# Performance work log

Hardware: AMD Instinct MI355X
Metric: run time of the kernel (lower is better)

The kernel has to match this reference:

```python
import jax, jax.numpy as jnp
import numpy as np
import math

LN_EPS = 1e-5

def layer_norm(x, g, b):
    m = jnp.mean(x, axis=-1, keepdims=True)
    v = jnp.mean((x - m) ** 2, axis=-1, keepdims=True)
    return (x - m) / jnp.sqrt(v + LN_EPS) * g + b

def setup_inputs() -> dict:
    key = jax.random.key(0)
    ks = jax.random.split(key, 8)
    B, H, W, C = 64, 24, 24, 768   # ViT-B/16 @ 384 -> 576 tokens
    SD, N = 512, 8192              # sd_dim, FDT codebook size
    ft = jax.random.normal(ks[0], (B, H, W, C), jnp.float32)
    sd = jax.random.normal(ks[1], (N, SD), jnp.float32)
    mask = jax.random.randint(ks[2], (B, H * W), 0, 2, jnp.int32)
    inp = {
        "ft": ft,
        "sd": sd,
        "mask": mask,
        "ln1_g": jnp.ones((C,), jnp.float32),
        "ln1_b": jnp.zeros((C,), jnp.float32),
        "w1": jax.random.normal(ks[3], (C, SD), jnp.float32) * 0.02,
        "b1": jnp.zeros((SD,), jnp.float32),
        "ln2_g": jnp.ones((SD,), jnp.float32),
        "ln2_b": jnp.zeros((SD,), jnp.float32),
        "w2": jax.random.normal(ks[4], (SD, SD), jnp.float32) * 0.02,
        "b2": jnp.zeros((SD,), jnp.float32),
    }
    return inp

def reference(ft, sd, mask, ln1_g, ln1_b, w1, b1, ln2_g, ln2_b, w2, b2):
    B, H, W, C = ft.shape
    temperature = 1.0
    x = ft.reshape(B, H * W, C)                     # [B, T, C]
    # q_map: LN -> Linear -> GELU (exact, torch default) -> LN -> Linear
    q = layer_norm(x, ln1_g, ln1_b)
    q = q @ w1 + b1
    q = jax.nn.gelu(q, approximate=False)
    q = layer_norm(q, ln2_g, ln2_b)
    q = q @ w2 + b2                                  # [B, T, SD]
    att_dim = sd.shape[1]
    inner = jnp.einsum('btd,nd->btn', q, sd)         # [B, T, N]
    inner = inner / math.sqrt(att_dim)
    m = (mask == 0).astype(inner.dtype)              # [B, T]
    inner = inner * m[:, :, None]
    inner = inner / temperature
    pooled = inner.sum(axis=1)                       # sum pool over tokens -> [B, N]
    att_weight = jax.nn.softmax(pooled, axis=-1)     # [B, N]
    att_ft = att_weight @ sd                         # [B, SD]
    return (att_weight, att_ft, sd)
```

## Files before the change

kernel.cpp:

```cpp
#include <hip/hip_runtime.h>
#include <math.h>

typedef unsigned short u16;
typedef _Float16 half4 __attribute__((ext_vector_type(4)));
typedef _Float16 half8 __attribute__((ext_vector_type(8)));
typedef float f32x4 __attribute__((ext_vector_type(4)));
typedef u16 u16x8 __attribute__((ext_vector_type(8)));

#define B_ 64
#define T_ 576
#define C_ 768
#define SD_ 512
#define N_ 8192
#define TOK_ (B_*T_)
#define MT_ 5
#define HROWS_ 640

__device__ __forceinline__ u16 f2h(float x) {
    _Float16 v = (_Float16)x;
    return __builtin_bit_cast(u16, v);
}

__global__ void zero_kernel(unsigned int* attwh_u, unsigned int* qpad_u, int* count) {
    int i = blockIdx.x * 256 + threadIdx.x;
    if (i < 524288) attwh_u[i] = 0u;
    if (i < 16384)  qpad_u[i]  = 0u;
    if (i < 64)     count[i]   = 0;
}

__global__ __launch_bounds__(256) void transpose_cvt_kernel(
    const float* __restrict__ src, const float* __restrict__ g,
    u16* __restrict__ dst, int K, int N)
{
    __shared__ float tile[64][65];
    int k0 = blockIdx.x * 64, n0 = blockIdx.y * 64;
    int tid = threadIdx.x;
#pragma unroll
    for (int p = 0; p < 16; p++) {
        int idx = p * 256 + tid;
        int r = idx >> 6, c = idx & 63;
        float gv = g ? g[k0 + r] : 1.0f;
        tile[r][c] = src[(size_t)(k0 + r) * N + n0 + c] * gv;
    }
    __syncthreads();
#pragma unroll
    for (int p = 0; p < 16; p++) {
        int idx = p * 256 + tid;
        int r = idx >> 6, c = idx & 63;
        dst[(size_t)(n0 + r) * K + k0 + c] = f2h(tile[c][r]);
    }
}

__global__ void cvt_plain_kernel(const float* __restrict__ src, u16* __restrict__ dst) {
    int i = blockIdx.x * 256 + threadIdx.x;
    const f32x4* s = (const f32x4*)(src + (size_t)i * 8);
    f32x4 a = s[0], b = s[1];
    u16x8 o;
    o[0]=f2h(a[0]); o[1]=f2h(a[1]); o[2]=f2h(a[2]); o[3]=f2h(a[3]);
    o[4]=f2h(b[0]); o[5]=f2h(b[1]); o[6]=f2h(b[2]); o[7]=f2h(b[3]);
    *(u16x8*)(dst + (size_t)i * 8) = o;
}

__global__ void fold_bias_kernel(const float* __restrict__ w, const float* __restrict__ bvec,
                                 const float* __restrict__ beta, float* __restrict__ outp,
                                 int K, int N)
{
    int n = blockIdx.x, l = threadIdx.x;
    float s = 0.f;
    for (int k = l; k < K; k += 64) s += beta[k] * w[(size_t)k * N + n];
#pragma unroll
    for (int o = 32; o > 0; o >>= 1) s += __shfl_xor(s, o);
    if (l == 0) outp[n] = bvec[n] + s;
}

__global__ void compact_kernel(const int* __restrict__ mask, int* __restrict__ list,
                               int* __restrict__ count) {
    int g = blockIdx.x * 256 + threadIdx.x;
    if (g >= TOK_) return;
    int b = g / T_, t = g % T_;
    if (mask[g] == 0) {
        int slot = atomicAdd(&count[b], 1);
        list[b * T_ + slot] = t;
    }
}

__global__ void ln1_stats_kernel(const float* __restrict__ ft, const int* __restrict__ list,
                                 const int* __restrict__ count, float2* __restrict__ stats1) {
    int wv = threadIdx.x >> 6, lane = threadIdx.x & 63;
    int s = blockIdx.x * 4 + wv;
    int b = s / T_, slot = s % T_;
    if (slot >= count[b]) return;
    int t = list[b * T_ + slot];
    const float4* row = (const float4*)(ft + (size_t)(b * T_ + t) * C_);
    float sum = 0.f, sq = 0.f;
#pragma unroll
    for (int p = 0; p < 3; p++) {
        float4 v = row[lane + 64 * p];
        sum += (v.x + v.y) + (v.z + v.w);
        sq  += v.x * v.x + v.y * v.y + v.z * v.z + v.w * v.w;
    }
#pragma unroll
    for (int o = 32; o > 0; o >>= 1) { sum += __shfl_xor(sum, o); sq += __shfl_xor(sq, o); }
    if (lane == 0) {
        float mu  = sum * (1.0f / C_);
        float var = fmaxf(sq * (1.0f / C_) - mu * mu, 0.0f);
        stats1[b * T_ + slot] = make_float2(mu, 1.0f / sqrtf(var + 1e-5f));
    }
}

__global__ __launch_bounds__(256) void gemm1_kernel(
    const float* __restrict__ ft, const u16* __restrict__ w1T,
    const float* __restrict__ b1p, const int* __restrict__ list,
    const int* __restrict__ count, const float2* __restrict__ stats1,
    u16* __restrict__ h)
{
    const int b = blockIdx.x / MT_, mt = blockIdx.x % MT_;
    const int cnt = count[b];
    const int row0 = mt * 128;
    if (row0 >= cnt) return;
    const int n0 = blockIdx.y * 128;

    __shared__ __align__(16) u16 As[128 * 64];
    __shared__ __align__(16) u16 Bs[128 * 64];
    __shared__ float rmu[128], rrs[128];
    __shared__ int rtok[128];

    const int tid = threadIdx.x;
    if (tid < 128) {
        int slot = row0 + tid;
        bool v = slot < cnt;
        rtok[tid] = v ? list[b * T_ + slot] : 0;
        float2 st = v ? stats1[b * T_ + slot] : make_float2(0.f, 0.f);
        rmu[tid] = v ? st.x : 0.f;
        rrs[tid] = v ? st.y : 0.f;
    }
    __syncthreads();

    const float* aptr[4]; float amu[4], ars[4]; int adst[4];
    const u16* bptr[4];
#pragma unroll
    for (int it = 0; it < 4; it++) {
        int c = it * 256 + tid, r = c >> 3, q = c & 7;
        aptr[it] = ft + (size_t)(b * T_ + rtok[r]) * C_ + q * 8;
        amu[it] = rmu[r]; ars[it] = rrs[r];
        adst[it] = r * 64 + ((q ^ (r & 7)) << 3);
        bptr[it] = w1T + (size_t)(n0 + r) * C_ + q * 8;
    }

    const int lane = tid & 63, w = tid >> 6;
    const int wm = w >> 1, wn = w & 1;
    const int lr = lane & 15, lg = lane >> 4;
    int arow[4], brow[4];
#pragma unroll
    for (int i = 0; i < 4; i++) { arow[i] = wm * 64 + i * 16 + lr; brow[i] = wn * 64 + i * 16 + lr; }

    f32x4 pa0[4], pa1[4]; u16x8 pb[4];
#pragma unroll
    for (int it = 0; it < 4; it++) {
        pa0[it] = *(const f32x4*)(aptr[it]);
        pa1[it] = *(const f32x4*)(aptr[it] + 4);
        pb[it]  = *(const u16x8*)(bptr[it]);
    }

    f32x4 acc[4][4] = {};
    const int NKT = C_ / 64;
    for (int kt = 0; kt < NKT; kt++) {
        __syncthreads();
#pragma unroll
        for (int it = 0; it < 4; it++) {
            float mu = amu[it], rs = ars[it];
            u16x8 o;
            o[0] = f2h((pa0[it][0] - mu) * rs);
            o[1] = f2h((pa0[it][1] - mu) * rs);
            o[2] = f2h((pa0[it][2] - mu) * rs);
            o[3] = f2h((pa0[it][3] - mu) * rs);
            o[4] = f2h((pa1[it][0] - mu) * rs);
            o[5] = f2h((pa1[it][1] - mu) * rs);
            o[6] = f2h((pa1[it][2] - mu) * rs);
            o[7] = f2h((pa1[it][3] - mu) * rs);
            *(u16x8*)&As[adst[it]] = o;
            *(u16x8*)&Bs[adst[it]] = pb[it];
        }
        __syncthreads();
        if (kt + 1 < NKT) {
            int k = (kt + 1) * 64;
#pragma unroll
            for (int it = 0; it < 4; it++) {
                pa0[it] = *(const f32x4*)(aptr[it] + k);
                pa1[it] = *(const f32x4*)(aptr[it] + k + 4);
                pb[it]  = *(const u16x8*)(bptr[it] + k);
            }
        }
#pragma unroll
        for (int ks = 0; ks < 4; ks++) {
            int kq = ks * 4 + lg;
            int qo = kq >> 1, ho = (kq & 1) << 2;
            half4 aF[4], bF[4];
#pragma unroll
            for (int i = 0; i < 4; i++)
                aF[i] = *(const half4*)&As[arow[i] * 64 + ((qo ^ (arow[i] & 7)) << 3) + ho];
#pragma unroll
            for (int i = 0; i < 4; i++)
                bF[i] = *(const half4*)&Bs[brow[i] * 64 + ((qo ^ (brow[i] & 7)) << 3) + ho];
#pragma unroll
            for (int mi = 0; mi < 4; mi++)
#pragma unroll
                for (int ni = 0; ni < 4; ni++)
                    acc[mi][ni] = __builtin_amdgcn_mfma_f32_16x16x16f16(aF[mi], bF[ni], acc[mi][ni], 0, 0, 0);
        }
    }

    float bb[4];
#pragma unroll
    for (int ni = 0; ni < 4; ni++) bb[ni] = b1p[n0 + wn * 64 + ni * 16 + lr];
#pragma unroll
    for (int mi = 0; mi < 4; mi++) {
#pragma unroll
        for (int r = 0; r < 4; r++) {
            int grow = row0 + wm * 64 + mi * 16 + 4 * lg + r;
            u16* hp = h + (size_t)(b * HROWS_ + grow) * SD_ + n0 + wn * 64 + lr;
#pragma unroll
            for (int ni = 0; ni < 4; ni++) {
                float x = acc[mi][ni][r] + bb[ni];
                float gel = 0.5f * x * (1.0f + erff(x * 0.70710678118654752f));
                hp[ni * 16] = f2h(gel);
            }
        }
    }
}

__global__ void ln2_stats_kernel(const u16* __restrict__ h, const int* __restrict__ count,
                                 float2* __restrict__ stats2) {
    int wv = threadIdx.x >> 6, lane = threadIdx.x & 63;
    int s = blockIdx.x * 4 + wv;
    int b = s / T_, slot = s % T_;
    if (slot >= count[b]) return;
    const half8* row = (const half8*)(h + (size_t)(b * HROWS_ + slot) * SD_);
    half8 v = row[lane];
    float sum = 0.f, sq = 0.f;
#pragma unroll
    for (int j = 0; j < 8; j++) { float f = (float)v[j]; sum += f; sq += f * f; }
#pragma unroll
    for (int o = 32; o > 0; o >>= 1) { sum += __shfl_xor(sum, o); sq += __shfl_xor(sq, o); }
    if (lane == 0) {
        float mu  = sum * (1.0f / SD_);
        float var = fmaxf(sq * (1.0f / SD_) - mu * mu, 0.0f);
        stats2[b * T_ + slot] = make_float2(mu, 1.0f / sqrtf(var + 1e-5f));
    }
}

__global__ __launch_bounds__(256) void gemm2_kernel(
    const u16* __restrict__ h, const u16* __restrict__ w2T,
    const int* __restrict__ count, const float2* __restrict__ stats2,
    float* __restrict__ partial)
{
    const int b = blockIdx.x / MT_, mt = blockIdx.x % MT_;
    const int cnt = count[b];
    const int row0 = mt * 128;
    if (row0 >= cnt) return;
    const int n0 = blockIdx.y * 128;

    __shared__ __align__(16) u16 As[128 * 64];
    __shared__ __align__(16) u16 Bs[128 * 64];
    __shared__ float rmu[128], rrs[128];
    __shared__ float redbuf[4][64];

    const int tid = threadIdx.x;
    if (tid < 128) {
        int slot = row0 + tid;
        bool v = slot < cnt;
        float2 st = v ? stats2[b * T_ + slot] : make_float2(0.f, 0.f);
        rmu[tid] = v ? st.x : 0.f;
        rrs[tid] = v ? st.y : 0.f;
    }
    __syncthreads();

    const u16* aptr[4]; float amu[4], ars[4]; int adst[4];
    const u16* bptr[4];
#pragma unroll
    for (int it = 0; it < 4; it++) {
        int c = it * 256 + tid, r = c >> 3, q = c & 7;
        aptr[it] = h + (size_t)(b * HROWS_ + row0 + r) * SD_ + q * 8;
        amu[it] = rmu[r]; ars[it] = rrs[r];
        adst[it] = r * 64 + ((q ^ (r & 7)) << 3);
        bptr[it] = w2T + (size_t)(n0 + r) * SD_ + q * 8;
    }

    const int lane = tid & 63, w = tid >> 6;
    const int wm = w >> 1, wn = w & 1;
    const int lr = lane & 15, lg = lane >> 4;
    int arow[4], brow[4];
#pragma unroll
    for (int i = 0; i < 4; i++) { arow[i] = wm * 64 + i * 16 + lr; brow[i] = wn * 64 + i * 16 + lr; }

    u16x8 pa[4], pb[4];
#pragma unroll
    for (int it = 0; it < 4; it++) {
        pa[it] = *(const u16x8*)(aptr[it]);
        pb[it] = *(const u16x8*)(bptr[it]);
    }

    f32x4 acc[4][4] = {};
    const int NKT = SD_ / 64;
    for (int kt = 0; kt < NKT; kt++) {
        __syncthreads();
#pragma unroll
        for (int it = 0; it < 4; it++) {
            float mu = amu[it], rs = ars[it];
            half8 hv = __builtin_bit_cast(half8, pa[it]);
            u16x8 o;
#pragma unroll
            for (int j = 0; j < 8; j++) o[j] = f2h(((float)hv[j] - mu) * rs);
            *(u16x8*)&As[adst[it]] = o;
            *(u16x8*)&Bs[adst[it]] = pb[it];
        }
        __syncthreads();
        if (kt + 1 < NKT) {
            int k = (kt + 1) * 64;
#pragma unroll
            for (int it = 0; it < 4; it++) {
                pa[it] = *(const u16x8*)(aptr[it] + k);
                pb[it] = *(const u16x8*)(bptr[it] + k);
            }
        }
#pragma unroll
        for (int ks = 0; ks < 4; ks++) {
            int kq = ks * 4 + lg;
            int qo = kq >> 1, ho = (kq & 1) << 2;
            half4 aF[4], bF[4];
#pragma unroll
            for (int i = 0; i < 4; i++)
                aF[i] = *(const half4*)&As[arow[i] * 64 + ((qo ^ (arow[i] & 7)) << 3) + ho];
#pragma unroll
            for (int i = 0; i < 4; i++)
                bF[i] = *(const half4*)&Bs[brow[i] * 64 + ((qo ^ (brow[i] & 7)) << 3) + ho];
#pragma unroll
            for (int mi = 0; mi < 4; mi++)
#pragma unroll
                for (int ni = 0; ni < 4; ni++)
                    acc[mi][ni] = __builtin_amdgcn_mfma_f32_16x16x16f16(aF[mi], bF[ni], acc[mi][ni], 0, 0, 0);
        }
    }

    float s[4];
#pragma unroll
    for (int ni = 0; ni < 4; ni++) {
        float t = 0.f;
#pragma unroll
        for (int mi = 0; mi < 4; mi++)
#pragma unroll
            for (int r = 0; r < 4; r++) t += acc[mi][ni][r];
        t += __shfl_xor(t, 16);
        t += __shfl_xor(t, 32);
        s[ni] = t;
    }
    if (lane < 16) {
#pragma unroll
        for (int ni = 0; ni < 4; ni++) redbuf[w][ni * 16 + lr] = s[ni];
    }
    __syncthreads();
    if (tid < 128) {
        int wn2 = tid >> 6, idx = tid & 63;
        float v = redbuf[wn2][idx] + redbuf[wn2 + 2][idx];
        partial[(size_t)(b * MT_ + mt) * SD_ + n0 + tid] = v;
    }
}

__global__ void qsum_reduce_kernel(const float* __restrict__ partial, const int* __restrict__ count,
                                   const float* __restrict__ b2p, u16* __restrict__ qsumh) {
    int i = blockIdx.x * 256 + threadIdx.x;
    int b = i >> 9, d = i & 511;
    int cnt = count[b];
    int mts = (cnt + 127) >> 7;
    float s = 0.f;
    for (int mt = 0; mt < mts; mt++) s += partial[(size_t)(b * MT_ + mt) * SD_ + d];
    s = (s + (float)cnt * b2p[d]) * 0.04419417382415922f;
    qsumh[i] = f2h(s);
}

__global__ __launch_bounds__(256) void gemm_plain_kernel(
    const u16* __restrict__ A, int ldA,
    const u16* __restrict__ BT, int ldBT,
    float* __restrict__ C, int ldC, int nkt)
{
    const int kz = blockIdx.x, nt = blockIdx.y;
    const int n0 = nt * 128;
    const int kbase = kz * nkt * 64;

    __shared__ __align__(16) u16 As[128 * 64];
    __shared__ __align__(16) u16 Bs[128 * 64];

    const int tid = threadIdx.x;
    const u16* aptr[4]; const u16* bptr[4]; int adst[4];
#pragma unroll
    for (int it = 0; it < 4; it++) {
        int c = it * 256 + tid, r = c >> 3, q = c & 7;
        aptr[it] = A  + (size_t)r * ldA + kbase + q * 8;
        bptr[it] = BT + (size_t)(n0 + r) * ldBT + kbase + q * 8;
        adst[it] = r * 64 + ((q ^ (r & 7)) << 3);
    }

    const int lane = tid & 63, w = tid >> 6;
    const int wm = w >> 1, wn = w & 1;
    const int lr = lane & 15, lg = lane >> 4;
    int arow[4], brow[4];
#pragma unroll
    for (int i = 0; i < 4; i++) { arow[i] = wm * 64 + i * 16 + lr; brow[i] = wn * 64 + i * 16 + lr; }

    u16x8 pa[4], pb[4];
#pragma unroll
    for (int it = 0; it < 4; it++) {
        pa[it] = *(const u16x8*)(aptr[it]);
        pb[it] = *(const u16x8*)(bptr[it]);
    }

    f32x4 acc[4][4] = {};
    for (int kt = 0; kt < nkt; kt++) {
        __syncthreads();
#pragma unroll
        for (int it = 0; it < 4; it++) {
            *(u16x8*)&As[adst[it]] = pa[it];
            *(u16x8*)&Bs[adst[it]] = pb[it];
        }
        __syncthreads();
        if (kt + 1 < nkt) {
            int k = (kt + 1) * 64;
#pragma unroll
            for (int it = 0; it < 4; it++) {
                pa[it] = *(const u16x8*)(aptr[it] + k);
                pb[it] = *(const u16x8*)(bptr[it] + k);
            }
        }
#pragma unroll
        for (int ks = 0; ks < 4; ks++) {
            int kq = ks * 4 + lg;
            int qo = kq >> 1, ho = (kq & 1) << 2;
            half4 aF[4], bF[4];
#pragma unroll
            for (int i = 0; i < 4; i++)
                aF[i] = *(const half4*)&As[arow[i] * 64 + ((qo ^ (arow[i] & 7)) << 3) + ho];
#pragma unroll
            for (int i = 0; i < 4; i++)
                bF[i] = *(const half4*)&Bs[brow[i] * 64 + ((qo ^ (brow[i] & 7)) << 3) + ho];
#pragma unroll
            for (int mi = 0; mi < 4; mi++)
#pragma unroll
                for (int ni = 0; ni < 4; ni++)
                    acc[mi][ni] = __builtin_amdgcn_mfma_f32_16x16x16f16(aF[mi], bF[ni], acc[mi][ni], 0, 0, 0);
        }
    }

    float* Cb = C + (size_t)kz * 128 * ldC + n0;
#pragma unroll
    for (int mi = 0; mi < 4; mi++)
#pragma unroll
        for (int r = 0; r < 4; r++) {
            int grow = wm * 64 + mi * 16 + 4 * lg + r;
#pragma unroll
            for (int ni = 0; ni < 4; ni++)
                Cb[(size_t)grow * ldC + wn * 64 + ni * 16 + lr] = acc[mi][ni][r];
        }
}

__global__ __launch_bounds__(256) void softmax_kernel(const float* __restrict__ pooled,
                                                      float* __restrict__ attw,
                                                      u16* __restrict__ attwh) {
    __shared__ float rowm[N_];
    __shared__ float red[4];
    int b = blockIdx.x, tid = threadIdx.x;
    const float4* src = (const float4*)(pooled + (size_t)b * N_);
    float mx = -3.4e38f;
#pragma unroll
    for (int p = 0; p < 8; p++) {
        float4 v = src[tid + 256 * p];
        *((float4*)&rowm[(tid + 256 * p) * 4]) = v;
        mx = fmaxf(fmaxf(fmaxf(v.x, v.y), fmaxf(v.z, v.w)), mx);
    }
#pragma unroll
    for (int o = 32; o > 0; o >>= 1) mx = fmaxf(mx, __shfl_xor(mx, o));
    if ((tid & 63) == 0) red[tid >> 6] = mx;
    __syncthreads();
    mx = fmaxf(fmaxf(red[0], red[1]), fmaxf(red[2], red[3]));
    __syncthreads();
    float s = 0.f;
    for (int p = 0; p < 8; p++) {
        int i4 = tid + 256 * p;
        float4 v = *((float4*)&rowm[i4 * 4]);
        v.x = expf(v.x - mx); v.y = expf(v.y - mx);
        v.z = expf(v.z - mx); v.w = expf(v.w - mx);
        *((float4*)&rowm[i4 * 4]) = v;
        s += (v.x + v.y) + (v.z + v.w);
    }
#pragma unroll
    for (int o = 32; o > 0; o >>= 1) s += __shfl_xor(s, o);
    if ((tid & 63) == 0) red[tid >> 6] = s;
    __syncthreads();
    s = ((red[0] + red[1]) + (red[2] + red[3]));
    float inv = 1.0f / s;
    float4* dst = (float4*)(attw + (size_t)b * N_);
    u16* dh = attwh + (size_t)b * N_;
    for (int p = 0; p < 8; p++) {
        int i4 = tid + 256 * p;
        float4 v = *((float4*)&rowm[i4 * 4]);
        v.x *= inv; v.y *= inv; v.z *= inv; v.w *= inv;
        dst[i4] = v;
        ushort4 pk;
        pk.x = f2h(v.x); pk.y = f2h(v.y); pk.z = f2h(v.z); pk.w = f2h(v.w);
        *(ushort4*)(dh + (size_t)i4 * 4) = pk;
    }
}

__global__ void attft_reduce_kernel(const float* __restrict__ p2, float* __restrict__ att_ft) {
    int i = blockIdx.x * 256 + threadIdx.x;
    int b = i >> 9, d = i & 511;
    float s = 0.f;
#pragma unroll
    for (int kz = 0; kz < 8; kz++) s += p2[(size_t)kz * 128 * SD_ + (size_t)b * SD_ + d];
    att_ft[i] = s;
}

extern "C" void kernel_launch(void* const* d_in, const int* in_sizes, int n_in,
                              void* d_out, int out_size, void* d_ws, size_t ws_size,
                              hipStream_t stream) {
    (void)in_sizes; (void)n_in; (void)out_size; (void)ws_size;
    const float* ft  = (const float*)d_in[0];
    const float* sd  = (const float*)d_in[1];
    const int*   mask= (const int*)d_in[2];
    const float* g1  = (const float*)d_in[3];
    const float* bl1 = (const float*)d_in[4];
    const float* w1  = (const float*)d_in[5];
    const float* b1  = (const float*)d_in[6];
    const float* g2  = (const float*)d_in[7];
    const float* bl2 = (const float*)d_in[8];
    const float* w2  = (const float*)d_in[9];
    const float* b2  = (const float*)d_in[10];
    float* out = (float*)d_out;
    char* W = (char*)d_ws;

    u16*    w1T    = (u16*)(W + 0);
    u16*    w2T    = (u16*)(W + 786432);
    u16*    sdh    = (u16*)(W + 1310720);
    u16*    sdT    = (u16*)(W + 9699328);
    float*  b1p    = (float*)(W + 18087936);
    float*  b2p    = (float*)(W + 18089984);
    int*    list   = (int*)(W + 18092032);
    int*    count  = (int*)(W + 18239488);
    float2* st1    = (float2*)(W + 18239744);
    float2* st2    = (float2*)(W + 18534656);
    u16*    h      = (u16*)(W + 18829568);
    float*  partial= (float*)(W + 60772608);
    u16*    qsumh  = (u16*)(W + 61427968);
    float*  pooled = (float*)(W + 61559040);
    u16*    attwh  = (u16*)(W + 65753344);
    float*  p2     = (float*)(W + 67850496);

    float* att_w  = out;
    float* att_ft = out + (size_t)B_ * N_;
    float* sd_out = out + (size_t)B_ * N_ + (size_t)B_ * SD_;

    zero_kernel<<<2048, 256, 0, stream>>>((unsigned int*)attwh, (unsigned int*)(qsumh + 64 * SD_), count);
    transpose_cvt_kernel<<<dim3(C_ / 64, SD_ / 64), 256, 0, stream>>>(w1, g1, w1T, C_, SD_);
    transpose_cvt_kernel<<<dim3(SD_ / 64, SD_ / 64), 256, 0, stream>>>(w2, g2, w2T, SD_, SD_);
    transpose_cvt_kernel<<<dim3(N_ / 64, SD_ / 64), 256, 0, stream>>>(sd, nullptr, sdT, N_, SD_);
    cvt_plain_kernel<<<2048, 256, 0, stream>>>(sd, sdh);
    fold_bias_kernel<<<SD_, 64, 0, stream>>>(w1, b1, bl1, b1p, C_, SD_);
    fold_bias_kernel<<<SD_, 64, 0, stream>>>(w2, b2, bl2, b2p, SD_, SD_);
    compact_kernel<<<144, 256, 0, stream>>>(mask, list, count);
    ln1_stats_kernel<<<TOK_ / 4, 256, 0, stream>>>(ft, list, count, st1);
    gemm1_kernel<<<dim3(B_ * MT_, 4), 256, 0, stream>>>(ft, w1T, b1p, list, count, st1, h);
    ln2_stats_kernel<<<TOK_ / 4, 256, 0, stream>>>(h, count, st2);
    gemm2_kernel<<<dim3(B_ * MT_, 4), 256, 0, stream>>>(h, w2T, count, st2, partial);
    qsum_reduce_kernel<<<128, 256, 0, stream>>>(partial, count, b2p, qsumh);
    gemm_plain_kernel<<<dim3(1, 64), 256, 0, stream>>>(qsumh, SD_, sdh, SD_, pooled, N_, 8);
    softmax_kernel<<<B_, 256, 0, stream>>>(pooled, att_w, attwh);
    gemm_plain_kernel<<<dim3(8, 4), 256, 0, stream>>>(attwh, N_, sdT, N_, p2, SD_, 16);
    attft_reduce_kernel<<<128, 256, 0, stream>>>(p2, att_ft);
    hipMemcpyAsync(sd_out, sd, (size_t)N_ * SD_ * sizeof(float), hipMemcpyDeviceToDevice, stream);
}
```

Measured before the change: 474.6 us.

## Fuse LN2 stats into GEMM1 epilogue, use 16x16x32 MFMA, merge sd prep

GEMM1's epilogue now computes per-row partial sums and sums of squares of the GELU output and writes them to a partials buffer. GEMM2 reduces these 8 partials to get the LayerNorm-2 mean and inverse std, so the separate ln2_stats pass that re-read h is gone. All three GEMM kernels switch from the 16x16x16 f16 MFMA with half4 fragments to the 16x16x32 variant with half8 LDS reads, halving the MFMA issue count and LDS load instructions per k-tile. The sd half conversion and transpose are merged into one kernel that reads sd once. In exchange there are extra shuffles in the GEMM1 epilogue, a larger workspace, and stats computed from fp32 GELU values rather than the fp16-rounded h.

```diff
diff --git a/kernel.cpp b/kernel.cpp
--- a/kernel.cpp
+++ b/kernel.cpp
@@ -2,7 +2,6 @@
 #include <math.h>
 
 typedef unsigned short u16;
-typedef _Float16 half4 __attribute__((ext_vector_type(4)));
 typedef _Float16 half8 __attribute__((ext_vector_type(8)));
 typedef float f32x4 __attribute__((ext_vector_type(4)));
 typedef u16 u16x8 __attribute__((ext_vector_type(8)));
@@ -51,14 +50,27 @@
     }
 }
 
-__global__ void cvt_plain_kernel(const float* __restrict__ src, u16* __restrict__ dst) {
-    int i = blockIdx.x * 256 + threadIdx.x;
-    const f32x4* s = (const f32x4*)(src + (size_t)i * 8);
-    f32x4 a = s[0], b = s[1];
-    u16x8 o;
-    o[0]=f2h(a[0]); o[1]=f2h(a[1]); o[2]=f2h(a[2]); o[3]=f2h(a[3]);
-    o[4]=f2h(b[0]); o[5]=f2h(b[1]); o[6]=f2h(b[2]); o[7]=f2h(b[3]);
-    *(u16x8*)(dst + (size_t)i * 8) = o;
+__global__ __launch_bounds__(256) void sd_prep_kernel(
+    const float* __restrict__ sd, u16* __restrict__ sdh, u16* __restrict__ sdT)
+{
+    __shared__ float tile[64][65];
+    int k0 = blockIdx.x * 64, n0 = blockIdx.y * 64;
+    int tid = threadIdx.x;
+#pragma unroll
+    for (int p = 0; p < 16; p++) {
+        int idx = p * 256 + tid;
+        int r = idx >> 6, c = idx & 63;
+        float v = sd[(size_t)(k0 + r) * SD_ + n0 + c];
+        tile[r][c] = v;
+        sdh[(size_t)(k0 + r) * SD_ + n0 + c] = f2h(v);
+    }
+    __syncthreads();
+#pragma unroll
+    for (int p = 0; p < 16; p++) {
+        int idx = p * 256 + tid;
+        int r = idx >> 6, c = idx & 63;
+        sdT[(size_t)(n0 + r) * N_ + k0 + c] = f2h(tile[c][r]);
+    }
 }
 
 __global__ void fold_bias_kernel(const float* __restrict__ w, const float* __restrict__ bvec,
@@ -112,7 +124,7 @@
     const float* __restrict__ ft, const u16* __restrict__ w1T,
     const float* __restrict__ b1p, const int* __restrict__ list,
     const int* __restrict__ count, const float2* __restrict__ stats1,
-    u16* __restrict__ h)
+    u16* __restrict__ h, float* __restrict__ rstat)
 {
     const int b = blockIdx.x / MT_, mt = blockIdx.x % MT_;
     const int cnt = count[b];
@@ -192,21 +204,23 @@
             }
         }
 #pragma unroll
-        for (int ks = 0; ks < 4; ks++) {
-            int kq = ks * 4 + lg;
-            int qo = kq >> 1, ho = (kq & 1) << 2;
-            half4 aF[4], bF[4];
-#pragma unroll
-            for (int i = 0; i < 4; i++)
-                aF[i] = *(const half4*)&As[arow[i] * 64 + ((qo ^ (arow[i] & 7)) << 3) + ho];
-#pragma unroll
-            for (int i = 0; i < 4; i++)
-                bF[i] = *(const half4*)&Bs[brow[i] * 64 + ((qo ^ (brow[i] & 7)) << 3) + ho];
+        for (int ks = 0; ks < 2; ks++) {
+            half8 aF[4], bF[4];
+#pragma unroll
+            for (int i = 0; i < 4; i++) {
+                int ra = arow[i];
+                aF[i] = *(const half8*)&As[ra * 64 + (((ks * 4 + lg) ^ (ra & 7)) << 3)];
+            }
+#pragma unroll
+            for (int i = 0; i < 4; i++) {
+                int rb = brow[i];
+                bF[i] = *(const half8*)&Bs[rb * 64 + (((ks * 4 + lg) ^ (rb & 7)) << 3)];
+            }
 #pragma unroll
             for (int mi = 0; mi < 4; mi++)
 #pragma unroll
                 for (int ni = 0; ni < 4; ni++)
-                    acc[mi][ni] = __builtin_amdgcn_mfma_f32_16x16x16f16(aF[mi], bF[ni], acc[mi][ni], 0, 0, 0);
+                    acc[mi][ni] = __builtin_amdgcn_mfma_f32_16x16x32_f16(aF[mi], bF[ni], acc[mi][ni], 0, 0, 0);
         }
     }
 
@@ -219,39 +233,27 @@
         for (int r = 0; r < 4; r++) {
             int grow = row0 + wm * 64 + mi * 16 + 4 * lg + r;
             u16* hp = h + (size_t)(b * HROWS_ + grow) * SD_ + n0 + wn * 64 + lr;
+            float s = 0.f, q = 0.f;
 #pragma unroll
             for (int ni = 0; ni < 4; ni++) {
                 float x = acc[mi][ni][r] + bb[ni];
                 float gel = 0.5f * x * (1.0f + erff(x * 0.70710678118654752f));
                 hp[ni * 16] = f2h(gel);
-            }
-        }
-    }
-}
-
-__global__ void ln2_stats_kernel(const u16* __restrict__ h, const int* __restrict__ count,
-                                 float2* __restrict__ stats2) {
-    int wv = threadIdx.x >> 6, lane = threadIdx.x & 63;
-    int s = blockIdx.x * 4 + wv;
-    int b = s / T_, slot = s % T_;
-    if (slot >= count[b]) return;
-    const half8* row = (const half8*)(h + (size_t)(b * HROWS_ + slot) * SD_);
-    half8 v = row[lane];
-    float sum = 0.f, sq = 0.f;
-#pragma unroll
-    for (int j = 0; j < 8; j++) { float f = (float)v[j]; sum += f; sq += f * f; }
-#pragma unroll
-    for (int o = 32; o > 0; o >>= 1) { sum += __shfl_xor(sum, o); sq += __shfl_xor(sq, o); }
-    if (lane == 0) {
-        float mu  = sum * (1.0f / SD_);
-        float var = fmaxf(sq * (1.0f / SD_) - mu * mu, 0.0f);
-        stats2[b * T_ + slot] = make_float2(mu, 1.0f / sqrtf(var + 1e-5f));
+                s += gel; q += gel * gel;
+            }
+            s += __shfl_xor(s, 1); s += __shfl_xor(s, 2); s += __shfl_xor(s, 4); s += __shfl_xor(s, 8);
+            q += __shfl_xor(q, 1); q += __shfl_xor(q, 2); q += __shfl_xor(q, 4); q += __shfl_xor(q, 8);
+            if (lr == 0) {
+                float* rp = rstat + ((size_t)((blockIdx.y * 2 + wn) * B_ + b) * HROWS_ + grow) * 2;
+                rp[0] = s; rp[1] = q;
+            }
+        }
     }
 }
 
 __global__ __launch_bounds__(256) void gemm2_kernel(
     const u16* __restrict__ h, const u16* __restrict__ w2T,
-    const int* __restrict__ count, const float2* __restrict__ stats2,
+    const int* __restrict__ count, const float* __restrict__ rstat,
     float* __restrict__ partial)
 {
     const int b = blockIdx.x / MT_, mt = blockIdx.x % MT_;
@@ -269,9 +271,20 @@
     if (tid < 128) {
         int slot = row0 + tid;
         bool v = slot < cnt;
-        float2 st = v ? stats2[b * T_ + slot] : make_float2(0.f, 0.f);
-        rmu[tid] = v ? st.x : 0.f;
-        rrs[tid] = v ? st.y : 0.f;
+        float mu = 0.f, rs = 0.f;
+        if (v) {
+            float s = 0.f, q = 0.f;
+            size_t ro = (size_t)(row0 + tid) * 2;
+#pragma unroll
+            for (int p = 0; p < 8; p++) {
+                const float* rp = rstat + ((size_t)(p * B_ + b) * HROWS_) * 2 + ro;
+                s += rp[0]; q += rp[1];
+            }
+            mu = s * (1.0f / SD_);
+            float var = fmaxf(q * (1.0f / SD_) - mu * mu, 0.0f);
+            rs = 1.0f / sqrtf(var + 1e-5f);
+        }
+        rmu[tid] = mu; rrs[tid] = rs;
     }
     __syncthreads();
 
@@ -307,10 +320,12 @@
 #pragma unroll
         for (int it = 0; it < 4; it++) {
             float mu = amu[it], rs = ars[it];
-            half8 hv = __builtin_bit_cast(half8, pa[it]);
             u16x8 o;
 #pragma unroll
-            for (int j = 0; j < 8; j++) o[j] = f2h(((float)hv[j] - mu) * rs);
+            for (int j = 0; j < 8; j++) {
+                _Float16 hv = __builtin_bit_cast(_Float16, (u16)pa[it][j]);
+                o[j] = f2h(((float)hv - mu) * rs);
+            }
             *(u16x8*)&As[adst[it]] = o;
             *(u16x8*)&Bs[adst[it]] = pb[it];
         }
@@ -324,21 +339,23 @@
             }
         }
 #pragma unroll
-        for (int ks = 0; ks < 4; ks++) {
-            int kq = ks * 4 + lg;
-            int qo = kq >> 1, ho = (kq & 1) << 2;
-            half4 aF[4], bF[4];
-#pragma unroll
-            for (int i = 0; i < 4; i++)
-                aF[i] = *(const half4*)&As[arow[i] * 64 + ((qo ^ (arow[i] & 7)) << 3) + ho];
-#pragma unroll
-            for (int i = 0; i < 4; i++)
-                bF[i] = *(const half4*)&Bs[brow[i] * 64 + ((qo ^ (brow[i] & 7)) << 3) + ho];
+        for (int ks = 0; ks < 2; ks++) {
+            half8 aF[4], bF[4];
+#pragma unroll
+            for (int i = 0; i < 4; i++) {
+                int ra = arow[i];
+                aF[i] = *(const half8*)&As[ra * 64 + (((ks * 4 + lg) ^ (ra & 7)) << 3)];
+            }
+#pragma unroll
+            for (int i = 0; i < 4; i++) {
+                int rb = brow[i];
+                bF[i] = *(const half8*)&Bs[rb * 64 + (((ks * 4 + lg) ^ (rb & 7)) << 3)];
+            }
 #pragma unroll
             for (int mi = 0; mi < 4; mi++)
 #pragma unroll
                 for (int ni = 0; ni < 4; ni++)
-                    acc[mi][ni] = __builtin_amdgcn_mfma_f32_16x16x16f16(aF[mi], bF[ni], acc[mi][ni], 0, 0, 0);
+                    acc[mi][ni] = __builtin_amdgcn_mfma_f32_16x16x32_f16(aF[mi], bF[ni], acc[mi][ni], 0, 0, 0);
         }
     }
 
@@ -432,21 +449,23 @@
             }
         }
 #pragma unroll
-        for (int ks = 0; ks < 4; ks++) {
-            int kq = ks * 4 + lg;
-            int qo = kq >> 1, ho = (kq & 1) << 2;
-            half4 aF[4], bF[4];
-#pragma unroll
-            for (int i = 0; i < 4; i++)
-                aF[i] = *(const half4*)&As[arow[i] * 64 + ((qo ^ (arow[i] & 7)) << 3) + ho];
-#pragma unroll
-            for (int i = 0; i < 4; i++)
-                bF[i] = *(const half4*)&Bs[brow[i] * 64 + ((qo ^ (brow[i] & 7)) << 3) + ho];
+        for (int ks = 0; ks < 2; ks++) {
+            half8 aF[4], bF[4];
+#pragma unroll
+            for (int i = 0; i < 4; i++) {
+                int ra = arow[i];
+                aF[i] = *(const half8*)&As[ra * 64 + (((ks * 4 + lg) ^ (ra & 7)) << 3)];
+            }
+#pragma unroll
+            for (int i = 0; i < 4; i++) {
+                int rb = brow[i];
+                bF[i] = *(const half8*)&Bs[rb * 64 + (((ks * 4 + lg) ^ (rb & 7)) << 3)];
+            }
 #pragma unroll
             for (int mi = 0; mi < 4; mi++)
 #pragma unroll
                 for (int ni = 0; ni < 4; ni++)
-                    acc[mi][ni] = __builtin_amdgcn_mfma_f32_16x16x16f16(aF[mi], bF[ni], acc[mi][ni], 0, 0, 0);
+                    acc[mi][ni] = __builtin_amdgcn_mfma_f32_16x16x32_f16(aF[mi], bF[ni], acc[mi][ni], 0, 0, 0);
         }
     }
 
@@ -546,13 +565,13 @@
     int*    list   = (int*)(W + 18092032);
     int*    count  = (int*)(W + 18239488);
     float2* st1    = (float2*)(W + 18239744);
-    float2* st2    = (float2*)(W + 18534656);
-    u16*    h      = (u16*)(W + 18829568);
-    float*  partial= (float*)(W + 60772608);
-    u16*    qsumh  = (u16*)(W + 61427968);
-    float*  pooled = (float*)(W + 61559040);
-    u16*    attwh  = (u16*)(W + 65753344);
-    float*  p2     = (float*)(W + 67850496);
+    float*  rstat  = (float*)(W + 18534656);
+    u16*    h      = (u16*)(W + 21156096);
+    float*  partial= (float*)(W + 63099136);
+    u16*    qsumh  = (u16*)(W + 63754496);
+    float*  pooled = (float*)(W + 63885568);
+    u16*    attwh  = (u16*)(W + 68079872);
+    float*  p2     = (float*)(W + 70177024);
 
     float* att_w  = out;
     float* att_ft = out + (size_t)B_ * N_;
@@ -561,15 +580,13 @@
     zero_kernel<<<2048, 256, 0, stream>>>((unsigned int*)attwh, (unsigned int*)(qsumh + 64 * SD_), count);
     transpose_cvt_kernel<<<dim3(C_ / 64, SD_ / 64), 256, 0, stream>>>(w1, g1, w1T, C_, SD_);
     transpose_cvt_kernel<<<dim3(SD_ / 64, SD_ / 64), 256, 0, stream>>>(w2, g2, w2T, SD_, SD_);
-    transpose_cvt_kernel<<<dim3(N_ / 64, SD_ / 64), 256, 0, stream>>>(sd, nullptr, sdT, N_, SD_);
-    cvt_plain_kernel<<<2048, 256, 0, stream>>>(sd, sdh);
+    sd_prep_kernel<<<dim3(N_ / 64, SD_ / 64), 256, 0, stream>>>(sd, sdh, sdT);
     fold_bias_kernel<<<SD_, 64, 0, stream>>>(w1, b1, bl1, b1p, C_, SD_);
     fold_bias_kernel<<<SD_, 64, 0, stream>>>(w2, b2, bl2, b2p, SD_, SD_);
     compact_kernel<<<144, 256, 0, stream>>>(mask, list, count);
     ln1_stats_kernel<<<TOK_ / 4, 256, 0, stream>>>(ft, list, count, st1);
-    gemm1_kernel<<<dim3(B_ * MT_, 4), 256, 0, stream>>>(ft, w1T, b1p, list, count, st1, h);
-    ln2_stats_kernel<<<TOK_ / 4, 256, 0, stream>>>(h, count, st2);
-    gemm2_kernel<<<dim3(B_ * MT_, 4), 256, 0, stream>>>(h, w2T, count, st2, partial);
+    gemm1_kernel<<<dim3(B_ * MT_, 4), 256, 0, stream>>>(ft, w1T, b1p, list, count, st1, h, rstat);
+    gemm2_kernel<<<dim3(B_ * MT_, 4), 256, 0, stream>>>(h, w2T, count, rstat, partial);
     qsum_reduce_kernel<<<128, 256, 0, stream>>>(partial, count, b2p, qsumh);
     gemm_plain_kernel<<<dim3(1, 64), 256, 0, stream>>>(qsumh, SD_, sdh, SD_, pooled, N_, 8);
     softmax_kernel<<<B_, 256, 0, stream>>>(pooled, att_w, attwh);
```

Measured after the change: 438.6 us. 1.08x faster.
